# Kernel optimization log

Measured on AMD Instinct MI355X. Metric: run time of the kernel, lower is better.

The kernel has to match this reference:

```python
import jax, jax.numpy as jnp
import numpy as np

N_NODES = 50000
N_EDGES = 800000
D = 96
L = 4
N_GRAPHS = 256
BN_EPS = 1e-5


def setup_inputs() -> dict:
    key = jax.random.key(0)
    ks = jax.random.split(key, 8)
    x = jax.random.normal(ks[0], (N_NODES, D), dtype=jnp.float32)
    edge_index = jax.random.randint(ks[1], (2, N_EDGES), 0, N_NODES, dtype=jnp.int32)
    batch = jnp.sort(jax.random.randint(ks[2], (N_NODES,), 0, N_GRAPHS, dtype=jnp.int32))
    # Stacked per-layer parameters (all layers are 96->96).
    W = jax.random.normal(ks[3], (L, D, D), dtype=jnp.float32) / np.sqrt(D)
    b = jnp.zeros((L, D), dtype=jnp.float32)
    gamma = jnp.ones((L, D), dtype=jnp.float32)
    beta = jnp.zeros((L, D), dtype=jnp.float32)
    return {"x": x, "edge_index": edge_index, "batch": batch,
            "W": W, "b": b, "gamma": gamma, "beta": beta}


def _gcn_norm(edge_index):
    # Add self loops and compute symmetric normalization (PyG gcn_norm).
    loops = jnp.arange(N_NODES, dtype=edge_index.dtype)
    src = jnp.concatenate([edge_index[0], loops])  # [E+N]
    dst = jnp.concatenate([edge_index[1], loops])
    deg = jax.ops.segment_sum(jnp.ones_like(dst, dtype=jnp.float32), dst,
                              num_segments=N_NODES)
    dis = jnp.where(deg > 0, jax.lax.rsqrt(jnp.maximum(deg, 1.0)), 0.0)
    norm = dis[src] * dis[dst]  # [E+N]
    return src, dst, norm


def reference(x, edge_index, batch, W, b, gamma, beta):
    src, dst, norm = _gcn_norm(edge_index)
    h = x
    for i in range(L):
        # GCNConv: linear transform, then normalized scatter-add aggregation.
        hw = h @ W[i]                                  # [N, D]
        agg = jax.ops.segment_sum(hw[src] * norm[:, None], dst,
                                  num_segments=N_NODES) + b[i]
        # BatchNorm1d over nodes (training-mode batch statistics, biased var).
        mu = jnp.mean(agg, axis=0)
        var = jnp.mean(jnp.square(agg - mu), axis=0)
        hn = (agg - mu) * jax.lax.rsqrt(var + BN_EPS) * gamma[i] + beta[i]
        h = jax.nn.relu(hn)
        # dropout is identity in eval / deterministic reference
    # global_mean_pool
    sums = jax.ops.segment_sum(h, batch, num_segments=N_GRAPHS)     # [G, D]
    cnt = jax.ops.segment_sum(jnp.ones((N_NODES,), jnp.float32), batch,
                              num_segments=N_GRAPHS)
    return sums / jnp.maximum(cnt, 1.0)[:, None]
```

## Files before the change

kernel.cpp:

```cpp
#include <hip/hip_runtime.h>
#include <hip/hip_bf16.h>
#include <hip/hip_fp16.h>

#define N_NODES 50000
#define N_EDGES 800000
#define DD 96
#define NLAYER 4
#define N_GRAPHS 256
#define BN_EPS 1e-5f
#define SLABS 8
#define SFEAT 12
#define NCHUNK 64
#define CHUNK_E (N_EDGES / NCHUNK)
#define NRANGE 4
#define RANGE_N 12544

enum : size_t {
  O_CNT    = 0,
  O_STATS  = O_CNT + N_NODES,
  O_POOL   = O_STATS + 4 * 192,
  O_GCNT   = O_POOL + N_GRAPHS * DD,
  ZERO_END = O_GCNT + N_GRAPHS,
  O_ROWPTR = ZERO_END,
  O_DIS    = O_ROWPTR + N_NODES + 1,
  O_BSUMS  = O_DIS + N_NODES,
  O_EDGE   = (O_BSUMS + 256 + 3) & ~size_t(3),
  O_HWH    = (O_EDGE + N_EDGES + 3) & ~size_t(3),
  O_PART   = O_HWH + (size_t)SLABS * N_NODES * SFEAT / 2,
  O_LOCC   = O_PART + (size_t)NCHUNK * N_NODES / 2,
  O_P      = O_LOCC + N_EDGES / 2,
  WS_ELEMS = O_P + (size_t)N_NODES * DD
};

__device__ __forceinline__ void atomAddF(float* p, float v) {
  unsafeAtomicAdd(p, v);
}

__device__ __forceinline__ float2 h2f(unsigned int u) {
  __half2 h = *(__half2*)&u;
  return __half22float2(h);
}

__global__ __launch_bounds__(256) void k_phist(const int* __restrict__ dst,
                                               unsigned short* __restrict__ part,
                                               unsigned short* __restrict__ locc) {
  __shared__ int hist[RANGE_N];
  const int b = blockIdx.x;
  const int tid = threadIdx.x;
  const int e0 = b * CHUNK_E, e1 = e0 + CHUNK_E;
  for (int r = 0; r < NRANGE; ++r) {
    const int r0 = r * RANGE_N;
    for (int i = tid; i < RANGE_N; i += 256) hist[i] = 0;
    __syncthreads();
    for (int e = e0 + tid; e < e1; e += 256) {
      unsigned rel = (unsigned)(dst[e] - r0);
      if (rel < RANGE_N) locc[e] = (unsigned short)atomicAdd(&hist[rel], 1);
    }
    __syncthreads();
    for (int i = tid; i < RANGE_N; i += 256) {
      int n = r0 + i;
      if (n < N_NODES) part[(size_t)b * N_NODES + n] = (unsigned short)hist[i];
    }
    __syncthreads();
  }
}

__global__ __launch_bounds__(256) void k_reduce(unsigned short* __restrict__ part,
                                                int* __restrict__ cnt,
                                                float* __restrict__ dis,
                                                int* __restrict__ bsums) {
  __shared__ int s[256];
  const int tid = threadIdx.x;
  const int n = blockIdx.x * 256 + tid;
  int run = 0;
  if (n < N_NODES) {
#pragma unroll 8
    for (int b = 0; b < NCHUNK; ++b) {
      size_t idx = (size_t)b * N_NODES + n;
      int t = part[idx];
      part[idx] = (unsigned short)run;
      run += t;
    }
    cnt[n] = run;
    dis[n] = rsqrtf((float)(run + 1));
  }
  s[tid] = (n < N_NODES) ? run : 0;
  __syncthreads();
  for (int off = 128; off > 0; off >>= 1) {
    if (tid < off) s[tid] += s[tid + off];
    __syncthreads();
  }
  if (tid == 0) bsums[blockIdx.x] = s[0];
}

__device__ __forceinline__ int lbound(const int* __restrict__ a, int v) {
  int lo = 0, hi = N_NODES;
  while (lo < hi) { int m = (lo + hi) >> 1; if (a[m] < v) lo = m + 1; else hi = m; }
  return lo;
}

__global__ __launch_bounds__(256) void k_scan_bsums(int* __restrict__ bsums, int nb,
                                                    int* __restrict__ rowptr,
                                                    const int* __restrict__ batch,
                                                    int* __restrict__ gcnt) {
  __shared__ int s[256];
  int tid = threadIdx.x;
  int v = (tid < nb) ? bsums[tid] : 0;
  s[tid] = v;
  __syncthreads();
  for (int off = 1; off < 256; off <<= 1) {
    int add = (tid >= off) ? s[tid - off] : 0;
    __syncthreads();
    s[tid] += add;
    __syncthreads();
  }
  if (tid < nb) bsums[tid] = s[tid] - v;
  if (tid == 255) rowptr[N_NODES] = s[255];
  gcnt[tid] = lbound(batch, tid + 1) - lbound(batch, tid);
}

__global__ __launch_bounds__(256) void k_scan_write(const int* __restrict__ cnt,
                                                    const int* __restrict__ bsums,
                                                    int* __restrict__ rowptr) {
  __shared__ int s[256];
  int i = blockIdx.x * 256 + threadIdx.x;
  int v = (i < N_NODES) ? cnt[i] : 0;
  s[threadIdx.x] = v;
  __syncthreads();
  for (int off = 1; off < 256; off <<= 1) {
    int x = 0;
    if (threadIdx.x >= off) x = s[threadIdx.x - off];
    __syncthreads();
    s[threadIdx.x] += x;
    __syncthreads();
  }
  if (i < N_NODES) rowptr[i] = bsums[blockIdx.x] + s[threadIdx.x] - v;
}

__global__ __launch_bounds__(256) void k_fill(const int* __restrict__ ei,
                                              const int* __restrict__ rowptr,
                                              const unsigned short* __restrict__ part,
                                              const unsigned short* __restrict__ locc,
                                              const float* __restrict__ dis,
                                              unsigned int* __restrict__ edg) {
  int e = blockIdx.x * 256 + threadIdx.x;
  if (e >= N_EDGES) return;
  int s = ei[e];
  int d = ei[N_EDGES + e];
  int chunk = e / CHUNK_E;
  int pos = rowptr[d] + (int)part[(size_t)chunk * N_NODES + d] + (int)locc[e];
  unsigned short wb = __half_as_ushort(__float2half_rn(dis[s] * dis[d]));
  edg[pos] = (unsigned int)s | ((unsigned int)wb << 16);
}

__global__ __launch_bounds__(192) void k_gemm(const float* __restrict__ X,
                                              const float* __restrict__ Wg,
                                              const float* __restrict__ stats,
                                              const float* __restrict__ gamma,
                                              const float* __restrict__ beta,
                                              __half* __restrict__ Y) {
  __shared__ float Ws[96 * 96];
  __shared__ float Hs[48][100];
  __shared__ float sA[96], sC[96];
  const int tid = threadIdx.x;
  const int fg = tid % 24;
  const int rg = tid / 24;
  const int row0 = blockIdx.x * 48;

  for (int i = tid; i < 96 * 24; i += 192)
    *(float4*)&Ws[i * 4] = *(const float4*)&Wg[i * 4];
  if (tid < 96) {
    if (stats) {
      float mu = stats[tid] * (1.f / N_NODES);
      float var = fmaxf(stats[96 + tid] * (1.f / N_NODES) - mu * mu, 0.f);
      float a = gamma[tid] * rsqrtf(var + BN_EPS);
      sA[tid] = a;
      sC[tid] = beta[tid] - mu * a;
    } else {
      sA[tid] = 1.f;
      sC[tid] = 0.f;
    }
  }
  __syncthreads();
  const bool bn = (stats != nullptr);
  for (int i = tid; i < 48 * 24; i += 192) {
    int r = i / 24, c4 = (i % 24) * 4;
    int gr = row0 + r;
    float4 v = (gr < N_NODES) ? *(const float4*)&X[(size_t)gr * 96 + c4]
                              : make_float4(0.f, 0.f, 0.f, 0.f);
    if (bn) {
      v.x = fmaxf(v.x * sA[c4] + sC[c4], 0.f);
      v.y = fmaxf(v.y * sA[c4 + 1] + sC[c4 + 1], 0.f);
      v.z = fmaxf(v.z * sA[c4 + 2] + sC[c4 + 2], 0.f);
      v.w = fmaxf(v.w * sA[c4 + 3] + sC[c4 + 3], 0.f);
    }
    *(float4*)&Hs[r][c4] = v;
  }
  __syncthreads();

  float4 acc[6];
#pragma unroll
  for (int j = 0; j < 6; ++j) acc[j] = make_float4(0.f, 0.f, 0.f, 0.f);
  const int f4 = fg * 4;
  for (int k4 = 0; k4 < 96; k4 += 4) {
    float4 w0 = *(const float4*)&Ws[(k4 + 0) * 96 + f4];
    float4 w1 = *(const float4*)&Ws[(k4 + 1) * 96 + f4];
    float4 w2 = *(const float4*)&Ws[(k4 + 2) * 96 + f4];
    float4 w3 = *(const float4*)&Ws[(k4 + 3) * 96 + f4];
#pragma unroll
    for (int j = 0; j < 6; ++j) {
      const float4 h = *(const float4*)&Hs[rg + j * 8][k4];
      acc[j].x += h.x * w0.x + h.y * w1.x + h.z * w2.x + h.w * w3.x;
      acc[j].y += h.x * w0.y + h.y * w1.y + h.z * w2.y + h.w * w3.y;
      acc[j].z += h.x * w0.z + h.y * w1.z + h.z * w2.z + h.w * w3.z;
      acc[j].w += h.x * w0.w + h.y * w1.w + h.z * w2.w + h.w * w3.w;
    }
  }
  const int slab = fg / 3;
  const int off = (fg % 3) * 4;
#pragma unroll
  for (int j = 0; j < 6; ++j) {
    int r = row0 + rg + j * 8;
    if (r < N_NODES) {
      union { uint2 u; __half2 h[2]; } pk;
      pk.h[0] = __floats2half2_rn(acc[j].x, acc[j].y);
      pk.h[1] = __floats2half2_rn(acc[j].z, acc[j].w);
      *(uint2*)&Y[((size_t)slab * N_NODES + r) * SFEAT + off] = pk.u;
    }
  }
}

__global__ __launch_bounds__(256) void k_gather(const __half* __restrict__ hwh,
                                                const int* __restrict__ rowptr,
                                                const unsigned int* __restrict__ edg,
                                                const float* __restrict__ dis,
                                                float* __restrict__ agg,
                                                float* __restrict__ stats) {
  __shared__ float sred[24];
  const int tid = threadIdx.x;
  const int slab = blockIdx.x & (SLABS - 1);
  const int chunk = blockIdx.x >> 3;
  const int wave = tid >> 6;
  const int lane = tid & 63;
  const int g = lane / 6;
  const int ch = lane - g * 6;
  const int n = chunk * 40 + wave * 10 + g;
  const bool valid = (g < 10) && (n < N_NODES);
  const int nc = valid ? n : 0;

  const unsigned int* slabU =
      (const unsigned int*)(hwh) + (size_t)slab * N_NODES * (SFEAT / 2);

  if (tid < 24) sred[tid] = 0.f;

  const int js = valid ? rowptr[nc] : 0;
  const int je = valid ? rowptr[nc + 1] : 0;

  float a0 = 0.f, a1 = 0.f;
  if (valid) {
    float dn = dis[nc];
    float s2 = dn * dn;
    float2 f = h2f(slabU[nc * 6 + ch]);
    a0 = f.x * s2;
    a1 = f.y * s2;
  }

  for (int j = js; j < je; j += 8) {
    unsigned int ew[8];
    unsigned int rv[8];
#pragma unroll
    for (int k = 0; k < 8; ++k) {
      int jk = j + k;
      int jc = jk < je ? jk : (je - 1);
      ew[k] = edg[jc];
    }
#pragma unroll
    for (int k = 0; k < 8; ++k)
      rv[k] = slabU[(int)(ew[k] & 0xFFFFu) * 6 + ch];
#pragma unroll
    for (int k = 0; k < 8; ++k) {
      float w = (j + k < je)
                    ? __half2float(__ushort_as_half((unsigned short)(ew[k] >> 16)))
                    : 0.f;
      float2 f = h2f(rv[k]);
      a0 = fmaf(w, f.x, a0);
      a1 = fmaf(w, f.y, a1);
    }
  }

  if (valid) {
    *(float2*)&agg[(size_t)n * DD + slab * SFEAT + ch * 2] = make_float2(a0, a1);
  }

  __syncthreads();
  if (valid) {
    atomicAdd(&sred[ch * 2], a0);
    atomicAdd(&sred[ch * 2 + 1], a1);
    atomicAdd(&sred[12 + ch * 2], a0 * a0);
    atomicAdd(&sred[13 + ch * 2], a1 * a1);
  }
  __syncthreads();
  if (tid < 24) {
    int c = (tid < 12) ? (slab * SFEAT + tid) : (96 + slab * SFEAT + tid - 12);
    atomAddF(&stats[c], sred[tid]);
  }
}

__global__ __launch_bounds__(192) void k_pool(const float* __restrict__ h,
                                              const float* __restrict__ stats,
                                              const float* __restrict__ gamma,
                                              const float* __restrict__ beta,
                                              const int* __restrict__ batch,
                                              float* __restrict__ pool) {
  __shared__ float sA[96], sC[96];
  const int tid = threadIdx.x;
  if (tid < 96) {
    float mu = stats[tid] * (1.f / N_NODES);
    float var = fmaxf(stats[96 + tid] * (1.f / N_NODES) - mu * mu, 0.f);
    float a = gamma[tid] * rsqrtf(var + BN_EPS);
    sA[tid] = a;
    sC[tid] = beta[tid] - mu * a;
  }
  __syncthreads();
  const int chain = blockIdx.x * 8 + tid / 24;
  const int q4 = (tid % 24) * 4;
  int n0 = chain * 32;
  if (n0 >= N_NODES) return;
  int n1 = min(n0 + 32, N_NODES);
  float A0 = sA[q4], A1 = sA[q4 + 1], A2 = sA[q4 + 2], A3 = sA[q4 + 3];
  float C0 = sC[q4], C1 = sC[q4 + 1], C2 = sC[q4 + 2], C3 = sC[q4 + 3];
  int cur = batch[n0];
  float4 acc = make_float4(0.f, 0.f, 0.f, 0.f);
  for (int n = n0; n < n1; ++n) {
    int g = batch[n];
    if (g != cur) {
      float* p = &pool[cur * 96 + q4];
      atomAddF(p, acc.x); atomAddF(p + 1, acc.y);
      atomAddF(p + 2, acc.z); atomAddF(p + 3, acc.w);
      acc = make_float4(0.f, 0.f, 0.f, 0.f);
      cur = g;
    }
    const float4 v = *(const float4*)&h[(size_t)n * 96 + q4];
    acc.x += fmaxf(v.x * A0 + C0, 0.f);
    acc.y += fmaxf(v.y * A1 + C1, 0.f);
    acc.z += fmaxf(v.z * A2 + C2, 0.f);
    acc.w += fmaxf(v.w * A3 + C3, 0.f);
  }
  float* p = &pool[cur * 96 + q4];
  atomAddF(p, acc.x); atomAddF(p + 1, acc.y);
  atomAddF(p + 2, acc.z); atomAddF(p + 3, acc.w);
}

__global__ void k_out(const float* __restrict__ pool, const int* __restrict__ gcnt,
                      float* __restrict__ out) {
  int t = blockIdx.x * blockDim.x + threadIdx.x;
  if (t >= N_GRAPHS * 96) return;
  int g = t / 96;
  int c = gcnt[g];
  if (c < 1) c = 1;
  out[t] = pool[t] / (float)c;
}

extern "C" void kernel_launch(void* const* d_in, const int* in_sizes, int n_in,
                              void* d_out, int out_size, void* d_ws, size_t ws_size,
                              hipStream_t stream) {
  const float* x     = (const float*)d_in[0];
  const int*   ei    = (const int*)d_in[1];
  const int*   batch = (const int*)d_in[2];
  const float* W     = (const float*)d_in[3];
  const float* gamma = (const float*)d_in[5];
  const float* beta  = (const float*)d_in[6];
  float* out = (float*)d_out;

  float* ws = (float*)d_ws;
  int*   cnt    = (int*)(ws + O_CNT);
  float* stats  = ws + O_STATS;
  float* pool   = ws + O_POOL;
  int*   gcnt   = (int*)(ws + O_GCNT);
  int*   rowptr = (int*)(ws + O_ROWPTR);
  float* dis    = ws + O_DIS;
  int*   bsums  = (int*)(ws + O_BSUMS);
  unsigned int* edg = (unsigned int*)(ws + O_EDGE);
  __half* hwh   = (__half*)(ws + O_HWH);
  unsigned short* part = (unsigned short*)(ws + O_PART);
  unsigned short* locc = (unsigned short*)(ws + O_LOCC);
  float* P      = ws + O_P;

  hipMemsetAsync(stats, 0, (ZERO_END - O_STATS) * sizeof(float), stream);

  const int eb = (N_EDGES + 255) / 256;
  const int nb = (N_NODES + 255) / 256;
  k_phist<<<NCHUNK, 256, 0, stream>>>(ei + N_EDGES, part, locc);
  k_reduce<<<nb, 256, 0, stream>>>(part, cnt, dis, bsums);
  k_scan_bsums<<<1, 256, 0, stream>>>(bsums, nb, rowptr, batch, gcnt);
  k_scan_write<<<nb, 256, 0, stream>>>(cnt, bsums, rowptr);
  k_fill<<<eb, 256, 0, stream>>>(ei, rowptr, part, locc, dis, edg);

  const int gemmb = (N_NODES + 47) / 48;
  const int gatherb = SLABS * ((N_NODES + 39) / 40);

  const float* hin = x;
  for (int l = 0; l < NLAYER; ++l) {
    const float* st = (l == 0) ? nullptr : (stats + (l - 1) * 192);
    const float* ga = (l == 0) ? nullptr : (gamma + (l - 1) * 96);
    const float* be = (l == 0) ? nullptr : (beta + (l - 1) * 96);
    k_gemm<<<gemmb, 192, 0, stream>>>(hin, W + l * 96 * 96, st, ga, be, hwh);
    k_gather<<<gatherb, 256, 0, stream>>>(hwh, rowptr, edg, dis, P, stats + l * 192);
    hin = P;
  }

  const int poolb = ((N_NODES + 31) / 32 + 7) / 8;
  k_pool<<<poolb, 192, 0, stream>>>(P, stats + 3 * 192, gamma + 3 * 96, beta + 3 * 96,
                                    batch, pool);
  k_out<<<(N_GRAPHS * 96 + 255) / 256, 256, 0, stream>>>(pool, gcnt, out);
}
```

Measured before the change: 602.7 us.

## Use MFMA fp16 for per-layer GEMM and pad gather slab rows to 32 bytes

The FP32 FMA GEMM is replaced with MFMA 16x16x32 f16 instructions. Inputs are converted to fp16 in shared memory, with W transposed. Results are staged through LDS and written out. The slab layout in the feature buffer is padded from 6 to 8 uint32 per node, so each node's row in a slab is 32-byte aligned for the gather. This raises GEMM throughput and gives the random gathers aligned rows, at the cost of rounding GEMM inputs to fp16 and about a third more feature-buffer footprint.

After: 576.1 us. -4.4%, faster.

```diff
diff --git a/kernel.cpp b/kernel.cpp
--- a/kernel.cpp
+++ b/kernel.cpp
@@ -10,10 +10,14 @@
 #define BN_EPS 1e-5f
 #define SLABS 8
 #define SFEAT 12
+#define GSU 8
 #define NCHUNK 64
 #define CHUNK_E (N_EDGES / NCHUNK)
 #define NRANGE 4
 #define RANGE_N 12544
+
+typedef _Float16 half8_t __attribute__((ext_vector_type(8)));
+typedef float floatx4 __attribute__((ext_vector_type(4)));
 
 enum : size_t {
   O_CNT    = 0,
@@ -24,9 +28,9 @@
   O_ROWPTR = ZERO_END,
   O_DIS    = O_ROWPTR + N_NODES + 1,
   O_BSUMS  = O_DIS + N_NODES,
-  O_EDGE   = (O_BSUMS + 256 + 3) & ~size_t(3),
-  O_HWH    = (O_EDGE + N_EDGES + 3) & ~size_t(3),
-  O_PART   = O_HWH + (size_t)SLABS * N_NODES * SFEAT / 2,
+  O_EDGE   = (O_BSUMS + 256 + 7) & ~size_t(7),
+  O_HWH    = (O_EDGE + N_EDGES + 7) & ~size_t(7),
+  O_PART   = O_HWH + (size_t)SLABS * N_NODES * GSU,
   O_LOCC   = O_PART + (size_t)NCHUNK * N_NODES / 2,
   O_P      = O_LOCC + N_EDGES / 2,
   WS_ELEMS = O_P + (size_t)N_NODES * DD
@@ -153,22 +157,18 @@
   edg[pos] = (unsigned int)s | ((unsigned int)wb << 16);
 }
 
-__global__ __launch_bounds__(192) void k_gemm(const float* __restrict__ X,
+__global__ __launch_bounds__(256) void k_gemm(const float* __restrict__ X,
                                               const float* __restrict__ Wg,
                                               const float* __restrict__ stats,
                                               const float* __restrict__ gamma,
                                               const float* __restrict__ beta,
-                                              __half* __restrict__ Y) {
-  __shared__ float Ws[96 * 96];
-  __shared__ float Hs[48][100];
+                                              unsigned int* __restrict__ Yu) {
+  __shared__ _Float16 Xh[64 * 104];
+  __shared__ _Float16 Wt[96 * 104];
   __shared__ float sA[96], sC[96];
   const int tid = threadIdx.x;
-  const int fg = tid % 24;
-  const int rg = tid / 24;
-  const int row0 = blockIdx.x * 48;
-
-  for (int i = tid; i < 96 * 24; i += 192)
-    *(float4*)&Ws[i * 4] = *(const float4*)&Wg[i * 4];
+  const int row0 = blockIdx.x * 64;
+
   if (tid < 96) {
     if (stats) {
       float mu = stats[tid] * (1.f / N_NODES);
@@ -181,9 +181,18 @@
       sC[tid] = 0.f;
     }
   }
+  for (int i = tid; i < 96 * 24; i += 256) {
+    int n = i / 24, k0 = (i % 24) * 4;
+    union { _Float16 h[4]; uint2 u; } pk;
+    pk.h[0] = (_Float16)Wg[(k0 + 0) * 96 + n];
+    pk.h[1] = (_Float16)Wg[(k0 + 1) * 96 + n];
+    pk.h[2] = (_Float16)Wg[(k0 + 2) * 96 + n];
+    pk.h[3] = (_Float16)Wg[(k0 + 3) * 96 + n];
+    *(uint2*)&Wt[n * 104 + k0] = pk.u;
+  }
   __syncthreads();
   const bool bn = (stats != nullptr);
-  for (int i = tid; i < 48 * 24; i += 192) {
+  for (int i = tid; i < 64 * 24; i += 256) {
     int r = i / 24, c4 = (i % 24) * 4;
     int gr = row0 + r;
     float4 v = (gr < N_NODES) ? *(const float4*)&X[(size_t)gr * 96 + c4]
@@ -194,43 +203,55 @@
       v.z = fmaxf(v.z * sA[c4 + 2] + sC[c4 + 2], 0.f);
       v.w = fmaxf(v.w * sA[c4 + 3] + sC[c4 + 3], 0.f);
     }
-    *(float4*)&Hs[r][c4] = v;
-  }
-  __syncthreads();
-
-  float4 acc[6];
-#pragma unroll
-  for (int j = 0; j < 6; ++j) acc[j] = make_float4(0.f, 0.f, 0.f, 0.f);
-  const int f4 = fg * 4;
-  for (int k4 = 0; k4 < 96; k4 += 4) {
-    float4 w0 = *(const float4*)&Ws[(k4 + 0) * 96 + f4];
-    float4 w1 = *(const float4*)&Ws[(k4 + 1) * 96 + f4];
-    float4 w2 = *(const float4*)&Ws[(k4 + 2) * 96 + f4];
-    float4 w3 = *(const float4*)&Ws[(k4 + 3) * 96 + f4];
-#pragma unroll
-    for (int j = 0; j < 6; ++j) {
-      const float4 h = *(const float4*)&Hs[rg + j * 8][k4];
-      acc[j].x += h.x * w0.x + h.y * w1.x + h.z * w2.x + h.w * w3.x;
-      acc[j].y += h.x * w0.y + h.y * w1.y + h.z * w2.y + h.w * w3.y;
-      acc[j].z += h.x * w0.z + h.y * w1.z + h.z * w2.z + h.w * w3.z;
-      acc[j].w += h.x * w0.w + h.y * w1.w + h.z * w2.w + h.w * w3.w;
-    }
-  }
-  const int slab = fg / 3;
-  const int off = (fg % 3) * 4;
-#pragma unroll
-  for (int j = 0; j < 6; ++j) {
-    int r = row0 + rg + j * 8;
-    if (r < N_NODES) {
-      union { uint2 u; __half2 h[2]; } pk;
-      pk.h[0] = __floats2half2_rn(acc[j].x, acc[j].y);
-      pk.h[1] = __floats2half2_rn(acc[j].z, acc[j].w);
-      *(uint2*)&Y[((size_t)slab * N_NODES + r) * SFEAT + off] = pk.u;
-    }
-  }
-}
-
-__global__ __launch_bounds__(256) void k_gather(const __half* __restrict__ hwh,
+    union { _Float16 h[4]; uint2 u; } pk;
+    pk.h[0] = (_Float16)v.x; pk.h[1] = (_Float16)v.y;
+    pk.h[2] = (_Float16)v.z; pk.h[3] = (_Float16)v.w;
+    *(uint2*)&Xh[r * 104 + c4] = pk.u;
+  }
+  __syncthreads();
+
+  const int w = tid >> 6, lane = tid & 63;
+  const int quad = lane >> 4, l16 = lane & 15;
+
+  half8_t a[3];
+#pragma unroll
+  for (int kb = 0; kb < 3; ++kb)
+    a[kb] = *(const half8_t*)&Xh[(w * 16 + l16) * 104 + kb * 32 + quad * 8];
+
+  floatx4 acc[6];
+#pragma unroll
+  for (int nt = 0; nt < 6; ++nt) acc[nt] = (floatx4){0.f, 0.f, 0.f, 0.f};
+#pragma unroll
+  for (int nt = 0; nt < 6; ++nt) {
+#pragma unroll
+    for (int kb = 0; kb < 3; ++kb) {
+      half8_t b = *(const half8_t*)&Wt[(nt * 16 + l16) * 104 + kb * 32 + quad * 8];
+      acc[nt] = __builtin_amdgcn_mfma_f32_16x16x32_f16(a[kb], b, acc[nt], 0, 0, 0);
+    }
+  }
+
+  __syncthreads();
+#pragma unroll
+  for (int nt = 0; nt < 6; ++nt) {
+#pragma unroll
+    for (int reg = 0; reg < 4; ++reg) {
+      int r = w * 16 + quad * 4 + reg;
+      Xh[r * 104 + nt * 16 + l16] = (_Float16)acc[nt][reg];
+    }
+  }
+  __syncthreads();
+  for (int i = tid; i < 64 * 24; i += 256) {
+    int r = i / 24, rem = i % 24;
+    int slab = rem / 3, up = rem % 3;
+    int node = row0 + r;
+    if (node < N_NODES) {
+      uint2 u = *(const uint2*)&Xh[r * 104 + slab * SFEAT + up * 4];
+      *(uint2*)&Yu[((size_t)slab * N_NODES + node) * GSU + up * 2] = u;
+    }
+  }
+}
+
+__global__ __launch_bounds__(256) void k_gather(const unsigned int* __restrict__ hw4,
                                                 const int* __restrict__ rowptr,
                                                 const unsigned int* __restrict__ edg,
                                                 const float* __restrict__ dis,
@@ -248,8 +269,7 @@
   const bool valid = (g < 10) && (n < N_NODES);
   const int nc = valid ? n : 0;
 
-  const unsigned int* slabU =
-      (const unsigned int*)(hwh) + (size_t)slab * N_NODES * (SFEAT / 2);
+  const unsigned int* slabU = hw4 + (size_t)slab * N_NODES * GSU;
 
   if (tid < 24) sred[tid] = 0.f;
 
@@ -260,7 +280,7 @@
   if (valid) {
     float dn = dis[nc];
     float s2 = dn * dn;
-    float2 f = h2f(slabU[nc * 6 + ch]);
+    float2 f = h2f(slabU[nc * GSU + ch]);
     a0 = f.x * s2;
     a1 = f.y * s2;
   }
@@ -276,7 +296,7 @@
     }
 #pragma unroll
     for (int k = 0; k < 8; ++k)
-      rv[k] = slabU[(int)(ew[k] & 0xFFFFu) * 6 + ch];
+      rv[k] = slabU[(size_t)(ew[k] & 0xFFFFu) * GSU + ch];
 #pragma unroll
     for (int k = 0; k < 8; ++k) {
       float w = (j + k < je)
@@ -381,7 +401,7 @@
   float* dis    = ws + O_DIS;
   int*   bsums  = (int*)(ws + O_BSUMS);
   unsigned int* edg = (unsigned int*)(ws + O_EDGE);
-  __half* hwh   = (__half*)(ws + O_HWH);
+  unsigned int* hw4 = (unsigned int*)(ws + O_HWH);
   unsigned short* part = (unsigned short*)(ws + O_PART);
   unsigned short* locc = (unsigned short*)(ws + O_LOCC);
   float* P      = ws + O_P;
@@ -396,7 +416,7 @@
   k_scan_write<<<nb, 256, 0, stream>>>(cnt, bsums, rowptr);
   k_fill<<<eb, 256, 0, stream>>>(ei, rowptr, part, locc, dis, edg);
 
-  const int gemmb = (N_NODES + 47) / 48;
+  const int gemmb = (N_NODES + 63) / 64;
   const int gatherb = SLABS * ((N_NODES + 39) / 40);
 
   const float* hin = x;
@@ -404,8 +424,8 @@
     const float* st = (l == 0) ? nullptr : (stats + (l - 1) * 192);
     const float* ga = (l == 0) ? nullptr : (gamma + (l - 1) * 96);
     const float* be = (l == 0) ? nullptr : (beta + (l - 1) * 96);
-    k_gemm<<<gemmb, 192, 0, stream>>>(hin, W + l * 96 * 96, st, ga, be, hwh);
-    k_gather<<<gatherb, 256, 0, stream>>>(hwh, rowptr, edg, dis, P, stats + l * 192);
+    k_gemm<<<gemmb, 256, 0, stream>>>(hin, W + l * 96 * 96, st, ga, be, hw4);
+    k_gather<<<gatherb, 256, 0, stream>>>(hw4, rowptr, edg, dis, P, stats + l * 192);
     hin = P;
   }
 
```
